# Kernel optimization log

Hardware: AMD Instinct MI355X
Metric: run time of the kernel (lower is better)

Reference implementation:

```python
import jax, jax.numpy as jnp
import numpy as np
import math

EMBED_DIM = 128
NUM_HEADS = 8
HDIM = EMBED_DIM // NUM_HEADS


def setup_inputs() -> dict:
    key = jax.random.key(0)
    kq, kh, km, k1, k2, k3, k4 = jax.random.split(key, 7)
    B, NQ, GS = 32, 1024, 1024
    q = jax.random.normal(kq, (B, NQ, EMBED_DIM), dtype=jnp.float32)
    h = jax.random.normal(kh, (B, GS, EMBED_DIM), dtype=jnp.float32)
    mask = jax.random.bernoulli(km, 0.15, (B, NQ, GS))
    stdv = 1.0 / math.sqrt(HDIM)
    Wq = jax.random.uniform(k1, (NUM_HEADS, EMBED_DIM, HDIM), jnp.float32, -stdv, stdv)
    Wk = jax.random.uniform(k2, (NUM_HEADS, EMBED_DIM, HDIM), jnp.float32, -stdv, stdv)
    Wv = jax.random.uniform(k3, (NUM_HEADS, EMBED_DIM, HDIM), jnp.float32, -stdv, stdv)
    stdv_o = 1.0 / math.sqrt(EMBED_DIM)
    Wout = jax.random.uniform(k4, (NUM_HEADS, HDIM, EMBED_DIM), jnp.float32, -stdv_o, stdv_o)
    return {"q": q, "h": h, "mask": mask, "Wq": Wq, "Wk": Wk, "Wv": Wv, "Wout": Wout}


def reference(q, h, mask, Wq, Wk, Wv, Wout):
    norm = 1.0 / math.sqrt(HDIM)
    # per-head projections: [h, b, n, e]
    Q = jnp.einsum('bnd,hde->hbne', q, Wq)
    K = jnp.einsum('bgd,hde->hbge', h, Wk)
    V = jnp.einsum('bgd,hde->hbge', h, Wv)
    compat = norm * jnp.einsum('hbne,hbge->hbng', Q, K)  # [h,b,nq,gs]
    m = mask[None]  # broadcast over heads
    compat = jnp.where(m, -jnp.inf, compat)
    attn = jax.nn.softmax(compat, axis=-1)
    attn = jnp.where(m, 0.0, attn)
    heads = jnp.einsum('hbng,hbge->hbne', attn, V)
    out = jnp.einsum('hbne,hed->bnd', heads, Wout)
    return out
```

## Files before the change

kernel.cpp:

```cpp
#include <hip/hip_runtime.h>

typedef unsigned short u16;
typedef unsigned int   u32;
typedef short bf16x8 __attribute__((ext_vector_type(8)));
typedef float f32x4  __attribute__((ext_vector_type(4)));

#define NB  32
#define NQ  1024
#define GS  1024
#define NH  8
#define SCQ (0.25f * 1.4426950408889634f)

#define MFMA16(a, b, c) __builtin_amdgcn_mfma_f32_16x16x32_bf16(a, b, c, 0, 0, 0)

__device__ __forceinline__ u16 f2bf(float f) {
    u32 u = __float_as_uint(f);
    return (u16)((u + 0x7fffu + ((u >> 16) & 1u)) >> 16);
}
__device__ __forceinline__ u32 pk2bf(float a, float b) {
    u32 ua = (__float_as_uint(a) + 0x8000u) >> 16;
    u32 ub = (__float_as_uint(b) + 0x8000u) & 0xffff0000u;
    return ua | ub;
}

template <int MODE, int AIN, int WMODE>
__device__ __forceinline__ void mgemm(const void* __restrict__ Ain,
                                      const float* __restrict__ Wsrc,
                                      float wscale,
                                      float* __restrict__ outf,
                                      u16* __restrict__ outb,
                                      u16* As, u16* Ws, int row0) {
    const int t    = threadIdx.x;
    const int wv   = t >> 6;
    const int lane = t & 63;
    const int quad = lane >> 4;
    const int c    = lane & 15;

#pragma unroll
    for (int g0 = 0; g0 < 2048; g0 += 256) {
        int g = g0 + t;
        int row = g >> 4, k0 = (g & 15) * 8;
        if (AIN == 0) {
            const float4* ap =
                (const float4*)&((const float*)Ain)[(size_t)(row0 + row) * 128 + k0];
            float4 a0 = ap[0], a1 = ap[1];
            int4 pk;
            pk.x = (int)pk2bf(a0.x, a0.y);
            pk.y = (int)pk2bf(a0.z, a0.w);
            pk.z = (int)pk2bf(a1.x, a1.y);
            pk.w = (int)pk2bf(a1.z, a1.w);
            *(int4*)&As[row * 136 + k0] = pk;
        } else {
            *(int4*)&As[row * 136 + k0] =
                *(const int4*)&((const u16*)Ain)[(size_t)(row0 + row) * 128 + k0];
        }
    }
#pragma unroll
    for (int i0 = 0; i0 < 16384; i0 += 256) {
        int i = i0 + t;
        float v = Wsrc[i];
        if (WMODE == 0) {
            int hh = i >> 11, d = (i >> 4) & 127, e = i & 15;
            Ws[(hh * 16 + e) * 136 + d] = f2bf(v * wscale);
        } else {
            int he = i >> 7, d = i & 127;
            Ws[d * 136 + he] = f2bf(v);
        }
    }
    __syncthreads();

    const f32x4 zf = {0.f, 0.f, 0.f, 0.f};
    f32x4 acc[2][8];
#pragma unroll
    for (int s = 0; s < 2; ++s)
#pragma unroll
        for (int j = 0; j < 8; ++j) acc[s][j] = zf;

#pragma unroll
    for (int kt = 0; kt < 4; ++kt) {
        bf16x8 af0 = *(const bf16x8*)&As[(wv * 32 + c) * 136 + kt * 32 + quad * 8];
        bf16x8 af1 = *(const bf16x8*)&As[(wv * 32 + 16 + c) * 136 + kt * 32 + quad * 8];
#pragma unroll
        for (int j = 0; j < 8; ++j) {
            bf16x8 bfr = *(const bf16x8*)&Ws[(j * 16 + c) * 136 + kt * 32 + quad * 8];
            acc[0][j] = MFMA16(af0, bfr, acc[0][j]);
            acc[1][j] = MFMA16(af1, bfr, acc[1][j]);
        }
    }

#pragma unroll
    for (int s = 0; s < 2; ++s)
#pragma unroll
        for (int j = 0; j < 8; ++j)
#pragma unroll
            for (int r = 0; r < 4; ++r) {
                int row = row0 + wv * 32 + s * 16 + quad * 4 + r;
                int col = j * 16 + c;
                float v = acc[s][j][r];
                if (MODE == 0) {
                    outb[(size_t)row * 128 + col] = f2bf(v);
                } else if (MODE == 2) {
                    int bI = row >> 10, tb = row & 1023;
                    outb[(size_t)bI * (128 * 1024) + (size_t)col * 1024 + tb] = f2bf(v);
                } else {
                    outf[(size_t)row * 128 + col] = v;
                }
            }
}

__global__ __launch_bounds__(256, 2) void proj_mfma(const float* __restrict__ q,
                                                    const float* __restrict__ h,
                                                    const float* __restrict__ Wq,
                                                    const float* __restrict__ Wk,
                                                    const float* __restrict__ Wv,
                                                    u16* __restrict__ Qb,
                                                    u16* __restrict__ Kb,
                                                    u16* __restrict__ Vtg) {
    __shared__ u16 As[128 * 136];
    __shared__ u16 Ws[128 * 136];
    int row0 = blockIdx.x * 128;
    if (blockIdx.y == 0)      mgemm<0, 0, 0>(q, Wq, SCQ,  nullptr, Qb,  As, Ws, row0);
    else if (blockIdx.y == 1) mgemm<0, 0, 0>(h, Wk, 1.0f, nullptr, Kb,  As, Ws, row0);
    else                      mgemm<2, 0, 0>(h, Wv, 1.0f, nullptr, Vtg, As, Ws, row0);
}

__global__ __launch_bounds__(256, 2) void outproj_mfma(const u16* __restrict__ headsb,
                                                       const float* __restrict__ Wout,
                                                       float* __restrict__ out) {
    __shared__ u16 As[128 * 136];
    __shared__ u16 Ws[128 * 136];
    mgemm<1, 1, 1>(headsb, Wout, 1.0f, out, nullptr, As, Ws, blockIdx.x * 128);
}

__global__ __launch_bounds__(512, 4) void flash_mfma(const u16* __restrict__ Qb,
                                                     const u16* __restrict__ Kb,
                                                     const u16* __restrict__ Vtg,
                                                     const int* __restrict__ mask,
                                                     u16* __restrict__ headsb) {
    __shared__ u16 Kt[32 * 136];
    __shared__ u16 Vtt[128 * 36];
    __shared__ u16 Ps[NH][32 * 36];
    __shared__ int Mt[32 * 34];

    const int b    = blockIdx.x;
    const int q0   = blockIdx.y * 32;
    const int t    = threadIdx.x;
    const int hh   = t >> 6;
    const int lane = t & 63;
    const int quad = lane >> 4;
    const int c    = lane & 15;

    const f32x4  zf = {0.f, 0.f, 0.f, 0.f};
    const bf16x8 zb = {0, 0, 0, 0, 0, 0, 0, 0};

    bf16x8 qf[2];
#pragma unroll
    for (int s = 0; s < 2; ++s) {
        qf[s] = zb;
        if (quad < 2)
            qf[s] = *(const bf16x8*)&Qb[((size_t)b * NQ + q0 + s * 16 + c) * 128 +
                                        hh * 16 + quad * 8];
    }

    f32x4 O[2] = {zf, zf};
    float ls[2][4] = {{0.f, 0.f, 0.f, 0.f}, {0.f, 0.f, 0.f, 0.f}};

    const int skey = t >> 4;
    const int sd0  = (t & 15) * 8;
    const int vdim = t >> 2;
    const int vk0  = (t & 3) * 8;
    const int mrow = t >> 4;
    const int mk0  = (t & 15) * 2;

    const u16* Kbase = &Kb[((size_t)b * GS + skey) * 128 + sd0];
    const u16* Vbase = &Vtg[(size_t)b * (128 * 1024) + (size_t)vdim * 1024 + vk0];
    const int* Mbase = &mask[((size_t)b * NQ + q0 + mrow) * GS + mk0];

    int4 kreg = *(const int4*)Kbase;
    int4 vreg = *(const int4*)Vbase;
    int2 mreg = *(const int2*)Mbase;

    for (int g0 = 0; g0 < GS; g0 += 32) {
        __syncthreads();
        *(int4*)&Kt[skey * 136 + sd0] = kreg;
        *(int4*)&Vtt[vdim * 36 + vk0] = vreg;
        *(int2*)&Mt[mrow * 34 + mk0]  = mreg;
        __syncthreads();

        if (g0 + 32 < GS) {
            kreg = *(const int4*)(Kbase + (size_t)(g0 + 32) * 128);
            vreg = *(const int4*)(Vbase + (g0 + 32));
            mreg = *(const int2*)(Mbase + (g0 + 32));
        }

        f32x4 sc[2][2];
#pragma unroll
        for (int kt = 0; kt < 2; ++kt) {
            bf16x8 kf = zb;
            if (quad < 2)
                kf = *(const bf16x8*)&Kt[(kt * 16 + c) * 136 + hh * 16 + quad * 8];
            sc[0][kt] = MFMA16(qf[0], kf, zf);
            sc[1][kt] = MFMA16(qf[1], kf, zf);
        }
        bf16x8 vf = *(const bf16x8*)&Vtt[(hh * 16 + c) * 36 + quad * 8];

#pragma unroll
        for (int s = 0; s < 2; ++s) {
#pragma unroll
            for (int r = 0; r < 4; ++r) {
                int mtrow = (s * 16 + quad * 4 + r) * 34;
                int m0 = Mt[mtrow + c];
                int m1 = Mt[mtrow + 16 + c];
                float e0 = exp2f(sc[s][0][r]);
                float e1 = exp2f(sc[s][1][r]);
                e0 = m0 ? 0.f : e0;
                e1 = m1 ? 0.f : e1;
                ls[s][r] += e0 + e1;
                u32 u0 = __float_as_uint(e0) + 0x8000u;
                u32 u1 = __float_as_uint(e1) + 0x8000u;
                int row = s * 16 + quad * 4 + r;
                Ps[hh][row * 36 + c]      = (u16)(u0 >> 16);
                Ps[hh][row * 36 + 16 + c] = (u16)(u1 >> 16);
            }
        }

#pragma unroll
        for (int s = 0; s < 2; ++s) {
            bf16x8 pf = *(const bf16x8*)&Ps[hh][(s * 16 + c) * 36 + quad * 8];
            O[s] = MFMA16(pf, vf, O[s]);
        }
    }

#pragma unroll
    for (int s = 0; s < 2; ++s)
#pragma unroll
        for (int r = 0; r < 4; ++r) {
            float l = ls[s][r];
            l += __shfl_xor(l, 1);
            l += __shfl_xor(l, 2);
            l += __shfl_xor(l, 4);
            l += __shfl_xor(l, 8);
            float rl = (l > 0.f) ? 1.f / l : 0.f;
            headsb[((size_t)b * NQ + q0 + s * 16 + quad * 4 + r) * 128 + hh * 16 + c] =
                f2bf(O[s][r] * rl);
        }
}

extern "C" void kernel_launch(void* const* d_in, const int* in_sizes, int n_in,
                              void* d_out, int out_size, void* d_ws, size_t ws_size,
                              hipStream_t stream) {
    const float* q    = (const float*)d_in[0];
    const float* h    = (const float*)d_in[1];
    const int*   mask = (const int*)d_in[2];
    const float* Wq   = (const float*)d_in[3];
    const float* Wk   = (const float*)d_in[4];
    const float* Wv   = (const float*)d_in[5];
    const float* Wout = (const float*)d_in[6];
    float* out = (float*)d_out;

    const size_t NTOK = (size_t)NB * NQ;
    u16* Qb  = (u16*)d_ws;
    u16* Kb  = Qb + NTOK * 128;
    u16* Vtg = Kb + NTOK * 128;
    u16* Hb  = Vtg + NTOK * 128;

    proj_mfma<<<dim3(256, 3), 256, 0, stream>>>(q, h, Wq, Wk, Wv, Qb, Kb, Vtg);
    flash_mfma<<<dim3(NB, NQ / 32), 512, 0, stream>>>(Qb, Kb, Vtg, mask, Hb);
    outproj_mfma<<<dim3(256, 1), 256, 0, stream>>>(Hb, Wout, out);
}
```

Before: 322.8 us.

## Fuse output projection into flash kernel and fold mask into MFMA accumulator

Removes the separate output-projection launch: the flash kernel stages normalized heads in shared memory and multiplies by a bf16 Wout, pre-converted by one projection block, writing fp32 output directly. The mask is converted into a -1e30 additive bias stored transposed in LDS and used as the score MFMA's initial accumulator, which removes the per-element select. Probability packing uses a paired bf16 convert, and the V tile load is split into two half loads that are interleaved in registers. This removes the heads round-trip through global memory and one launch, at the cost of extra work and synchronisation at the end of each flash block.

```diff
diff --git a/kernel.cpp b/kernel.cpp
--- a/kernel.cpp
+++ b/kernel.cpp
@@ -10,6 +10,7 @@
 #define GS  1024
 #define NH  8
 #define SCQ (0.25f * 1.4426950408889634f)
+#define MBIG (-1.0e30f)
 
 #define MFMA16(a, b, c) __builtin_amdgcn_mfma_f32_16x16x32_bf16(a, b, c, 0, 0, 0)
 
@@ -22,12 +23,21 @@
     u32 ub = (__float_as_uint(b) + 0x8000u) & 0xffff0000u;
     return ua | ub;
 }
-
-template <int MODE, int AIN, int WMODE>
-__device__ __forceinline__ void mgemm(const void* __restrict__ Ain,
+__device__ __forceinline__ u32 packbf2(float a, float b) {
+#if __has_builtin(__builtin_amdgcn_cvt_pk_bf16_f32)
+    auto pk = __builtin_amdgcn_cvt_pk_bf16_f32(a, b);
+    u32 w;
+    __builtin_memcpy(&w, &pk, 4);
+    return w;
+#else
+    return pk2bf(a, b);
+#endif
+}
+
+template <int MODE>
+__device__ __forceinline__ void mgemm(const float* __restrict__ Ain,
                                       const float* __restrict__ Wsrc,
                                       float wscale,
-                                      float* __restrict__ outf,
                                       u16* __restrict__ outb,
                                       u16* As, u16* Ws, int row0) {
     const int t    = threadIdx.x;
@@ -40,32 +50,21 @@
     for (int g0 = 0; g0 < 2048; g0 += 256) {
         int g = g0 + t;
         int row = g >> 4, k0 = (g & 15) * 8;
-        if (AIN == 0) {
-            const float4* ap =
-                (const float4*)&((const float*)Ain)[(size_t)(row0 + row) * 128 + k0];
-            float4 a0 = ap[0], a1 = ap[1];
-            int4 pk;
-            pk.x = (int)pk2bf(a0.x, a0.y);
-            pk.y = (int)pk2bf(a0.z, a0.w);
-            pk.z = (int)pk2bf(a1.x, a1.y);
-            pk.w = (int)pk2bf(a1.z, a1.w);
-            *(int4*)&As[row * 136 + k0] = pk;
-        } else {
-            *(int4*)&As[row * 136 + k0] =
-                *(const int4*)&((const u16*)Ain)[(size_t)(row0 + row) * 128 + k0];
-        }
+        const float4* ap = (const float4*)&Ain[(size_t)(row0 + row) * 128 + k0];
+        float4 a0 = ap[0], a1 = ap[1];
+        int4 pk;
+        pk.x = (int)pk2bf(a0.x, a0.y);
+        pk.y = (int)pk2bf(a0.z, a0.w);
+        pk.z = (int)pk2bf(a1.x, a1.y);
+        pk.w = (int)pk2bf(a1.z, a1.w);
+        *(int4*)&As[row * 136 + k0] = pk;
     }
 #pragma unroll
     for (int i0 = 0; i0 < 16384; i0 += 256) {
         int i = i0 + t;
         float v = Wsrc[i];
-        if (WMODE == 0) {
-            int hh = i >> 11, d = (i >> 4) & 127, e = i & 15;
-            Ws[(hh * 16 + e) * 136 + d] = f2bf(v * wscale);
-        } else {
-            int he = i >> 7, d = i & 127;
-            Ws[d * 136 + he] = f2bf(v);
-        }
+        int hh = i >> 11, d = (i >> 4) & 127, e = i & 15;
+        Ws[(hh * 16 + e) * 136 + d] = f2bf(v * wscale);
     }
     __syncthreads();
 
@@ -99,11 +98,9 @@
                 float v = acc[s][j][r];
                 if (MODE == 0) {
                     outb[(size_t)row * 128 + col] = f2bf(v);
-                } else if (MODE == 2) {
+                } else {
                     int bI = row >> 10, tb = row & 1023;
                     outb[(size_t)bI * (128 * 1024) + (size_t)col * 1024 + tb] = f2bf(v);
-                } else {
-                    outf[(size_t)row * 128 + col] = v;
                 }
             }
 }
@@ -113,34 +110,35 @@
                                                     const float* __restrict__ Wq,
                                                     const float* __restrict__ Wk,
                                                     const float* __restrict__ Wv,
+                                                    const float* __restrict__ Wout,
                                                     u16* __restrict__ Qb,
                                                     u16* __restrict__ Kb,
-                                                    u16* __restrict__ Vtg) {
+                                                    u16* __restrict__ Vtg,
+                                                    u16* __restrict__ Wob) {
     __shared__ u16 As[128 * 136];
     __shared__ u16 Ws[128 * 136];
     int row0 = blockIdx.x * 128;
-    if (blockIdx.y == 0)      mgemm<0, 0, 0>(q, Wq, SCQ,  nullptr, Qb,  As, Ws, row0);
-    else if (blockIdx.y == 1) mgemm<0, 0, 0>(h, Wk, 1.0f, nullptr, Kb,  As, Ws, row0);
-    else                      mgemm<2, 0, 0>(h, Wv, 1.0f, nullptr, Vtg, As, Ws, row0);
-}
-
-__global__ __launch_bounds__(256, 2) void outproj_mfma(const u16* __restrict__ headsb,
-                                                       const float* __restrict__ Wout,
-                                                       float* __restrict__ out) {
-    __shared__ u16 As[128 * 136];
-    __shared__ u16 Ws[128 * 136];
-    mgemm<1, 1, 1>(headsb, Wout, 1.0f, out, nullptr, As, Ws, blockIdx.x * 128);
+    if (blockIdx.y == 0 && blockIdx.x == 0) {
+        for (int i = threadIdx.x; i < 16384; i += 256) {
+            int d = i >> 7, k = i & 127, hh = k >> 4, e = k & 15;
+            Wob[i] = f2bf(Wout[hh * 2048 + e * 128 + d]);
+        }
+    }
+    if (blockIdx.y == 0)      mgemm<0>(q, Wq, SCQ,  Qb,  As, Ws, row0);
+    else if (blockIdx.y == 1) mgemm<0>(h, Wk, 1.0f, Kb,  As, Ws, row0);
+    else                      mgemm<2>(h, Wv, 1.0f, Vtg, As, Ws, row0);
 }
 
 __global__ __launch_bounds__(512, 4) void flash_mfma(const u16* __restrict__ Qb,
                                                      const u16* __restrict__ Kb,
                                                      const u16* __restrict__ Vtg,
                                                      const int* __restrict__ mask,
-                                                     u16* __restrict__ headsb) {
+                                                     const u16* __restrict__ Wob,
+                                                     float* __restrict__ out) {
     __shared__ u16 Kt[32 * 136];
     __shared__ u16 Vtt[128 * 36];
     __shared__ u16 Ps[NH][32 * 36];
-    __shared__ int Mt[32 * 34];
+    __shared__ float Mf[32 * 36];
 
     const int b    = blockIdx.x;
     const int q0   = blockIdx.y * 32;
@@ -168,28 +166,38 @@
     const int skey = t >> 4;
     const int sd0  = (t & 15) * 8;
     const int vdim = t >> 2;
-    const int vk0  = (t & 3) * 8;
+    const int vq   = t & 3;
     const int mrow = t >> 4;
     const int mk0  = (t & 15) * 2;
 
     const u16* Kbase = &Kb[((size_t)b * GS + skey) * 128 + sd0];
-    const u16* Vbase = &Vtg[(size_t)b * (128 * 1024) + (size_t)vdim * 1024 + vk0];
+    const u16* Vbase = &Vtg[(size_t)b * (128 * 1024) + (size_t)vdim * 1024];
     const int* Mbase = &mask[((size_t)b * NQ + q0 + mrow) * GS + mk0];
 
     int4 kreg = *(const int4*)Kbase;
-    int4 vreg = *(const int4*)Vbase;
+    int2 va   = *(const int2*)(Vbase + vq * 4);
+    int2 vb   = *(const int2*)(Vbase + 16 + vq * 4);
     int2 mreg = *(const int2*)Mbase;
 
     for (int g0 = 0; g0 < GS; g0 += 32) {
         __syncthreads();
         *(int4*)&Kt[skey * 136 + sd0] = kreg;
-        *(int4*)&Vtt[vdim * 36 + vk0] = vreg;
-        *(int2*)&Mt[mrow * 34 + mk0]  = mreg;
+        {
+            int4 w;
+            w.x = (int)(((u32)va.x & 0xffffu) | ((u32)vb.x << 16));
+            w.y = (int)(((u32)va.x >> 16) | ((u32)vb.x & 0xffff0000u));
+            w.z = (int)(((u32)va.y & 0xffffu) | ((u32)vb.y << 16));
+            w.w = (int)(((u32)va.y >> 16) | ((u32)vb.y & 0xffff0000u));
+            *(int4*)&Vtt[vdim * 36 + vq * 8] = w;
+        }
+        Mf[mk0 * 36 + mrow]       = mreg.x ? MBIG : 0.f;
+        Mf[(mk0 + 1) * 36 + mrow] = mreg.y ? MBIG : 0.f;
         __syncthreads();
 
         if (g0 + 32 < GS) {
             kreg = *(const int4*)(Kbase + (size_t)(g0 + 32) * 128);
-            vreg = *(const int4*)(Vbase + (g0 + 32));
+            va   = *(const int2*)(Vbase + g0 + 32 + vq * 4);
+            vb   = *(const int2*)(Vbase + g0 + 48 + vq * 4);
             mreg = *(const int2*)(Mbase + (g0 + 32));
         }
 
@@ -199,8 +207,11 @@
             bf16x8 kf = zb;
             if (quad < 2)
                 kf = *(const bf16x8*)&Kt[(kt * 16 + c) * 136 + hh * 16 + quad * 8];
-            sc[0][kt] = MFMA16(qf[0], kf, zf);
-            sc[1][kt] = MFMA16(qf[1], kf, zf);
+#pragma unroll
+            for (int s = 0; s < 2; ++s) {
+                f32x4 c0 = *(const f32x4*)&Mf[(kt * 16 + c) * 36 + s * 16 + quad * 4];
+                sc[s][kt] = MFMA16(qf[s], kf, c0);
+            }
         }
         bf16x8 vf = *(const bf16x8*)&Vtt[(hh * 16 + c) * 36 + quad * 8];
 
@@ -208,19 +219,11 @@
         for (int s = 0; s < 2; ++s) {
 #pragma unroll
             for (int r = 0; r < 4; ++r) {
-                int mtrow = (s * 16 + quad * 4 + r) * 34;
-                int m0 = Mt[mtrow + c];
-                int m1 = Mt[mtrow + 16 + c];
                 float e0 = exp2f(sc[s][0][r]);
                 float e1 = exp2f(sc[s][1][r]);
-                e0 = m0 ? 0.f : e0;
-                e1 = m1 ? 0.f : e1;
                 ls[s][r] += e0 + e1;
-                u32 u0 = __float_as_uint(e0) + 0x8000u;
-                u32 u1 = __float_as_uint(e1) + 0x8000u;
                 int row = s * 16 + quad * 4 + r;
-                Ps[hh][row * 36 + c]      = (u16)(u0 >> 16);
-                Ps[hh][row * 36 + 16 + c] = (u16)(u1 >> 16);
+                *(u32*)&Ps[hh][row * 36 + 2 * c] = packbf2(e0, e1);
             }
         }
 
@@ -231,6 +234,7 @@
         }
     }
 
+    float rl[2][4];
 #pragma unroll
     for (int s = 0; s < 2; ++s)
 #pragma unroll
@@ -240,10 +244,33 @@
             l += __shfl_xor(l, 2);
             l += __shfl_xor(l, 4);
             l += __shfl_xor(l, 8);
-            float rl = (l > 0.f) ? 1.f / l : 0.f;
-            headsb[((size_t)b * NQ + q0 + s * 16 + quad * 4 + r) * 128 + hh * 16 + c] =
-                f2bf(O[s][r] * rl);
-        }
+            rl[s][r] = (l > 0.f) ? 1.f / l : 0.f;
+        }
+    __syncthreads();
+    u16* Hs = Kt;
+#pragma unroll
+    for (int s = 0; s < 2; ++s)
+#pragma unroll
+        for (int r = 0; r < 4; ++r)
+            Hs[(s * 16 + quad * 4 + r) * 136 + hh * 16 + c] = f2bf(O[s][r] * rl[s][r]);
+    __syncthreads();
+
+    f32x4 oacc[2] = {zf, zf};
+#pragma unroll
+    for (int kt = 0; kt < 4; ++kt) {
+        bf16x8 bfr = *(const bf16x8*)&Wob[(hh * 16 + c) * 128 + kt * 32 + quad * 8];
+#pragma unroll
+        for (int s = 0; s < 2; ++s) {
+            bf16x8 af = *(const bf16x8*)&Hs[(s * 16 + c) * 136 + kt * 32 + quad * 8];
+            oacc[s] = MFMA16(af, bfr, oacc[s]);
+        }
+    }
+#pragma unroll
+    for (int s = 0; s < 2; ++s)
+#pragma unroll
+        for (int r = 0; r < 4; ++r)
+            out[((size_t)b * NQ + q0 + s * 16 + quad * 4 + r) * 128 + hh * 16 + c] =
+                oacc[s][r];
 }
 
 extern "C" void kernel_launch(void* const* d_in, const int* in_sizes, int n_in,
@@ -262,9 +289,9 @@
     u16* Qb  = (u16*)d_ws;
     u16* Kb  = Qb + NTOK * 128;
     u16* Vtg = Kb + NTOK * 128;
-    u16* Hb  = Vtg + NTOK * 128;
-
-    proj_mfma<<<dim3(256, 3), 256, 0, stream>>>(q, h, Wq, Wk, Wv, Qb, Kb, Vtg);
-    flash_mfma<<<dim3(NB, NQ / 32), 512, 0, stream>>>(Qb, Kb, Vtg, mask, Hb);
-    outproj_mfma<<<dim3(256, 1), 256, 0, stream>>>(Hb, Wout, out);
-}
+    u16* Wob = Vtg + NTOK * 128;
+
+    proj_mfma<<<dim3(256, 3), 256, 0, stream>>>(q, h, Wq, Wk, Wv, Wout,
+                                                Qb, Kb, Vtg, Wob);
+    flash_mfma<<<dim3(NB, NQ / 32), 512, 0, stream>>>(Qb, Kb, Vtg, mask, Wob, out);
+}
```

After: 322.8 us. No clear change (-0.0%).
